# Performance work log

Hardware: AMD Instinct MI355X
Metric: run time of the kernel (lower is better)

## Reference

```python
import jax, jax.numpy as jnp
import numpy as np

B, N = 16384, 20
F = 128          # n_node_features = n_neighbors_features = embed_dim
T = 100          # time_dim
E = 128          # n_edge_features
H = 2            # n_head
OUT = 128        # output_dimension
KEY_DIM = F + T + E  # 356


def setup_inputs() -> dict:
    key = jax.random.key(0)
    ks = jax.random.split(key, 24)
    s = 0.02
    inp = {
        "src_node_features": jax.random.normal(ks[0], (B, F), jnp.float32),
        "neighbors_features": jax.random.normal(ks[1], (B, N, F), jnp.float32),
        "neighbors_time_features": jax.random.normal(ks[2], (B, N, T), jnp.float32),
        "edge_features": jax.random.normal(ks[3], (B, N, E), jnp.float32),
        "neighbors_padding_mask": jax.random.randint(ks[4], (B, N), 0, 2).astype(bool),
        "weights": jax.random.uniform(ks[5], (B, N), jnp.float32),
        # transform: Linear(key_dim -> F)
        "Wt": jax.random.normal(ks[6], (F, KEY_DIM), jnp.float32) * s,
        "bt": jnp.zeros((F,), jnp.float32),
        # MultiheadAttention projections (embed_dim = kdim = vdim = F)
        "Wq": jax.random.normal(ks[7], (F, F), jnp.float32) * s,
        "bq": jnp.zeros((F,), jnp.float32),
        "Wk": jax.random.normal(ks[8], (F, F), jnp.float32) * s,
        "bk": jnp.zeros((F,), jnp.float32),
        "Wv": jax.random.normal(ks[9], (F, F), jnp.float32) * s,
        "bv": jnp.zeros((F,), jnp.float32),
        "Wo": jax.random.normal(ks[10], (F, F), jnp.float32) * s,
        "bo": jnp.zeros((F,), jnp.float32),
        # MergeLayer: fc1(query_dim + F -> F), fc2(F -> OUT)
        "W1": jax.random.normal(ks[11], (F, F + F), jnp.float32) * s,
        "b1": jnp.zeros((F,), jnp.float32),
        "W2": jax.random.normal(ks[12], (OUT, F), jnp.float32) * s,
        "b2": jnp.zeros((OUT,), jnp.float32),
    }
    return inp


def _gat_forward(src, nbr, timef, edgef, w, mask,
                 Wt, bt, Wq, bq, Wk, bk, Wv, bv, Wo, bo, W1, b1, W2, b2):
    b, f = src.shape
    dh = f // H
    scale = 1.0 / jnp.sqrt(jnp.asarray(dh, src.dtype))
    # key = transform(cat([nbr, edge, time])) * weights  -> [B,N,F]
    k_in = jnp.concatenate([nbr, edgef, timef], axis=2)
    keyv = (jnp.einsum('bnk,fk->bnf', k_in, Wt) + bt) * w[:, :, None]
    # invalid-neighborhood fixup: rows fully padded get their first slot unmasked
    invalid = mask.all(axis=1, keepdims=True)           # [B,1]
    mask = mask.at[:, 0].set(jnp.where(invalid[:, 0], False, mask[:, 0]))
    # projections (query_len = 1)
    q = (src @ Wq.T + bq).reshape(b, H, dh)             # [B,H,dh]
    k = (keyv @ Wk.T + bk).reshape(b, N, H, dh)         # [B,N,H,dh]
    v = (keyv @ Wv.T + bv).reshape(b, N, H, dh)
    scores = jnp.einsum('bhd,bnhd->bhn', q, k) * scale  # [B,H,N]
    scores = jnp.where(mask[:, None, :], -jnp.inf, scores)
    attn = jax.nn.softmax(scores, axis=-1)
    ctx = jnp.einsum('bhn,bnhd->bhd', attn, v).reshape(b, f)
    out = ctx @ Wo.T + bo                               # [B,F]
    out = jnp.where(invalid, jnp.asarray(0.0, out.dtype), out)
    out = jax.nn.relu(out)
    # MergeLayer: fc2(relu(fc1(cat([attn_out, src]))))
    hmid = jax.nn.relu(jnp.concatenate([out, src], axis=1) @ W1.T + b1)
    return hmid @ W2.T + b2


def reference(src_node_features, neighbors_features, neighbors_time_features,
              edge_features, neighbors_padding_mask, weights,
              Wt, bt, Wq, bq, Wk, bk, Wv, bv, Wo, bo, W1, b1, W2, b2):
    return _gat_forward(src_node_features, neighbors_features,
                        neighbors_time_features, edge_features, weights,
                        neighbors_padding_mask,
                        Wt, bt, Wq, bq, Wk, bk, Wv, bv, Wo, bo, W1, b1, W2, b2)
```

## Files before the change

### kernel.cpp

```cpp
#include <hip/hip_runtime.h>
#include <math.h>

#define NN 20
#define FF 128
#define TT 100
#define EE 128
#define KD 356

typedef unsigned int u32;
typedef unsigned short u16;
typedef unsigned long long u64;
typedef __attribute__((ext_vector_type(4))) float f32x4;
typedef __attribute__((ext_vector_type(8))) short s16x8;
typedef __attribute__((ext_vector_type(4))) u32 u32x4;

__device__ __forceinline__ u16 f2b(float f) {
    u32 u = __float_as_uint(f);
    u32 r = u + 0x7FFFu + ((u >> 16) & 1u);
    return (u16)(r >> 16);
}
__device__ __forceinline__ float b2f(u16 h) { return __uint_as_float(((u32)h) << 16); }
__device__ __forceinline__ float blo(u32 u){ return __uint_as_float(u << 16); }
__device__ __forceinline__ float bhi(u32 u){ return __uint_as_float(u & 0xFFFF0000u); }
__device__ __forceinline__ u32 pk2(float a, float b){ return (u32)f2b(a) | ((u32)f2b(b) << 16); }
__device__ __forceinline__ u32 cvtpk(float a, float b){
    u32 d; asm("v_cvt_pk_bf16_f32 %0, %1, %2" : "=v"(d) : "v"(a), "v"(b)); return d;
}


__global__ void prep_fuse(const float* __restrict__ Wt, const float* __restrict__ bt,
                          const float* __restrict__ Wk, const float* __restrict__ Wv,
                          const u32* __restrict__ maskw,
                          float* __restrict__ wkt, float* __restrict__ wvt,
                          float* __restrict__ kfb, float* __restrict__ vfb, int* __restrict__ flagp)
{
    const int blk = blockIdx.x, t = threadIdx.x;
    if (blk < KD) {
        __shared__ float col[FF];
        col[t] = Wt[t * KD + blk];
        __syncthreads();
        float ak = 0.f, av = 0.f;
        for (int j = 0; j < FF; ++j) {
            float c = col[j];
            ak = fmaf(Wk[t * FF + j], c, ak);
            av = fmaf(Wv[t * FF + j], c, av);
        }
        wkt[blk * FF + t] = ak;
        wvt[blk * FF + t] = av;
    } else if (blk == KD) {
        float ak = 0.f, av = 0.f;
        for (int j = 0; j < FF; ++j) {
            float c = bt[j];
            ak = fmaf(Wk[t * FF + j], c, ak);
            av = fmaf(Wv[t * FF + j], c, av);
        }
        kfb[t] = ak; vfb[t] = av;
    } else {
        int any = 0;
        for (int i = t; i < 8192; i += 128) any |= (maskw[i] > 1u) ? 1 : 0;
        any = __any(any) ? 1 : 0;
        __shared__ int red[2];
        if ((t & 63) == 0) red[t >> 6] = any;
        __syncthreads();
        if (t == 0) *flagp = (red[0] | red[1]) ? 1 : 0;
    }
}

__global__ void prep_pack_v4(const float* __restrict__ wkt, const float* __restrict__ wvt,
                             const float* __restrict__ Wq, const float* __restrict__ Wo,
                             const float* __restrict__ W1, const float* __restrict__ W2,
                             u16* __restrict__ kvB, u16* __restrict__ wqI, u16* __restrict__ woI,
                             u16* __restrict__ w1I, u16* __restrict__ w2I)
{
    const int id = blockIdx.x * 256 + threadIdx.x;
    if (id < 196608) {
        int chunk = id >> 9, e = id & 511;
        int ln = e >> 3, ee = e & 7;
        int kt = chunk >> 4, nb = chunk & 15;
        int k = kt * 32 + (ln >> 4) * 8 + ee;
        int n = nb * 16 + (ln & 15);
        float v = 0.f;
        if (k < KD) v = (n < FF) ? wkt[k * FF + n] : wvt[k * FF + (n - FF)];
        kvB[id] = f2b(v);
    } else if (id < 215040) {
        int e = id - 196608; int rem = e % 9216;
        int n = rem / 72, kk = rem % 72; int k = (e / 9216) * 64 + kk;
        wqI[e] = f2b(kk < 64 ? Wq[n * FF + k] : 0.f);
    } else if (id < 233472) {
        int e = id - 215040; int rem = e % 9216;
        int n = rem / 72, kk = rem % 72; int k = (e / 9216) * 64 + kk;
        woI[e] = f2b(kk < 64 ? Wo[n * FF + k] : 0.f);
    } else if (id < 270336) {
        int e = id - 233472; int rem = e % 9216;
        int n = rem / 72, kk = rem % 72; int k = (e / 9216) * 64 + kk;
        w1I[e] = f2b(kk < 64 ? W1[n * 2 * FF + k] : 0.f);
    } else if (id < 288768) {
        int e = id - 270336; int rem = e % 9216;
        int n = rem / 72, kk = rem % 72; int k = (e / 9216) * 64 + kk;
        w2I[e] = f2b(kk < 64 ? W2[n * FF + k] : 0.f);
    }
}

__global__ __launch_bounds__(512) void kv_attn_fused7(
    const float* __restrict__ nbr, const float* __restrict__ edg, const float* __restrict__ tmf,
    const float* __restrict__ wgt, const float* __restrict__ bk, const float* __restrict__ bv,
    const u16* __restrict__ kvB, const float* __restrict__ kfb, const float* __restrict__ vfb,
    const u16* __restrict__ Qg, const void* __restrict__ maskp, const int* __restrict__ flagp,
    u16* __restrict__ ctxout, unsigned char* __restrict__ flags)
{
    __shared__ __align__(16) u16 smem[15680];
    char* sb = (char*)smem;
    float* p_lds = (float*)(sb + 30720);
    u16* kls = (u16*)sb;

    const int tid = threadIdx.x;
    const int lane = tid & 63, wave = tid >> 6;
    const int wn = wave;
    const int Mbase = blockIdx.x * 80;
    const int Bbase = blockIdx.x * 4;
    const int kg = lane >> 4, l16 = lane & 15;

    f32x4 acc[5][2] = {};
    s16x8 br[2][2];
    f32x4 tl[5];

    #define STAGE_CHUNK(C, KT) do {                                                         \
        int row_ = (C) * 8 + (lane >> 3);                                                   \
        int x_ = (lane & 7) ^ (row_ & 7);                                                   \
        const float* g_;                                                                    \
        if ((KT) < 4)      g_ = nbr + (size_t)(Mbase + row_) * 128 + (KT) * 32 + x_ * 4;    \
        else if ((KT) < 8) g_ = edg + (size_t)(Mbase + row_) * 128 + ((KT)-4) * 32 + x_ * 4;\
        else               g_ = tmf + (size_t)(Mbase + row_) * 100 + ((KT)-8) * 32 + x_ * 4;\
        __builtin_amdgcn_global_load_lds((const __attribute__((address_space(1))) u32*)g_,  \
            (__attribute__((address_space(3))) u32*)(sb + ((KT)%3)*10240 + (C)*1024), 16, 0, 0); \
    } while (0)

    #define STAGE(KT) do {                                                                  \
        STAGE_CHUNK(wave, KT);                                                              \
        if (wave < 2) STAGE_CHUNK(8 + wave, KT);                                            \
    } while (0)

    #define LOADB(KT) do {                                                                  \
        br[(KT)&1][0] = *(const s16x8*)(kvB + (size_t)((KT)*16 + wn*2 + 0)*512 + lane*8);   \
        br[(KT)&1][1] = *(const s16x8*)(kvB + (size_t)((KT)*16 + wn*2 + 1)*512 + lane*8);   \
    } while (0)

    #define NV1(KT) ((KT)==0?6:((KT)==1?8:((KT)==2?10:((KT)<=8?8:((KT)==9?7:6)))))
    #define NV2(KT) ((KT)==0?8:((KT)==1?10:((KT)==2?12:((KT)<=8?10:((KT)==9?8:6)))))

    #pragma unroll
    for (int mt = 0; mt < 5; ++mt)
        tl[mt] = *(const f32x4*)(tmf + (size_t)(Mbase + mt * 16 + l16) * 100 + 96);
    STAGE(0); STAGE(1); STAGE(2);
    LOADB(0); LOADB(1);

    #define GITER(KT) do {                                                                  \
        if ((KT) <= 10) {                                                                   \
            if (wave < 2) { asm volatile("s_waitcnt vmcnt(%0)" :: "i"(NV2(KT)) : "memory"); }\
            else          { asm volatile("s_waitcnt vmcnt(%0)" :: "i"(NV1(KT)) : "memory"); }\
            __builtin_amdgcn_s_barrier();                                                   \
            __builtin_amdgcn_sched_barrier(0);                                              \
        }                                                                                   \
        s16x8 af[5];                                                                        \
        _Pragma("unroll")                                                                   \
        for (int mt = 0; mt < 5; ++mt) {                                                    \
            f32x4 lo, hi;                                                                   \
            if ((KT) <= 10) {                                                               \
                int r_ = mt * 16 + l16; int sw_ = r_ & 7; int y0_ = kg * 2;                 \
                const char* bp_ = sb + ((KT)%3)*10240 + r_ * 128;                           \
                lo = *(const f32x4*)(bp_ + ((y0_ ^ sw_) << 4));                             \
                hi = *(const f32x4*)(bp_ + (((y0_+1) ^ sw_) << 4));                         \
            } else {                                                                        \
                lo = (kg == 0) ? tl[mt] : (f32x4){0.f,0.f,0.f,0.f};                         \
                hi = (f32x4){0.f,0.f,0.f,0.f};                                              \
            }                                                                               \
            u32x4 q_;                                                                       \
            q_.x = cvtpk(lo.x, lo.y); q_.y = cvtpk(lo.z, lo.w);                             \
            q_.z = cvtpk(hi.x, hi.y); q_.w = cvtpk(hi.z, hi.w);                             \
            af[mt] = __builtin_bit_cast(s16x8, q_);                                         \
        }                                                                                   \
        _Pragma("unroll")                                                                   \
        for (int mt = 0; mt < 5; ++mt) {                                                    \
            acc[mt][0] = __builtin_amdgcn_mfma_f32_16x16x32_bf16(af[mt], br[(KT)&1][0], acc[mt][0], 0, 0, 0); \
            acc[mt][1] = __builtin_amdgcn_mfma_f32_16x16x32_bf16(af[mt], br[(KT)&1][1], acc[mt][1], 0, 0, 0); \
        }                                                                                   \
        if ((KT) <= 10) {                                                                   \
            asm volatile("s_waitcnt lgkmcnt(0)" ::: "memory");                              \
            __builtin_amdgcn_s_barrier();                                                   \
            __builtin_amdgcn_sched_barrier(0);                                              \
            if ((KT) <= 7) STAGE((KT)+3);                                                   \
            if ((KT)+2 <= 11) LOADB((KT)+2);                                                \
        }                                                                                   \
    } while (0)

    GITER(0); GITER(1); GITER(2);  GITER(3);
    GITER(4); GITER(5); GITER(6);  GITER(7);
    GITER(8); GITER(9); GITER(10); GITER(11);
    #undef GITER
    #undef STAGE
    #undef STAGE_CHUNK
    #undef LOADB

    __syncthreads();

    const int rg4 = (lane >> 4) * 4;
    if (wn < 4) {
        #pragma unroll
        for (int mt = 0; mt < 5; ++mt) {
            const int r0 = mt * 16 + rg4;
            float w4v[4];
            #pragma unroll
            for (int i = 0; i < 4; ++i) w4v[i] = wgt[Mbase + r0 + i];
            #pragma unroll
            for (int nt = 0; nt < 2; ++nt) {
                const int c = wn * 32 + nt * 16 + l16;
                const float fb = kfb[c], bb = bk[c];
                #pragma unroll
                for (int i = 0; i < 4; ++i)
                    kls[(r0 + i) * 132 + c] = f2b(fmaf(acc[mt][nt][i] + fb, w4v[i], bb));
            }
        }
    } else {
        #pragma unroll
        for (int mt = 0; mt < 5; ++mt) {
            const int r0 = mt * 16 + rg4;
            float w4v[4];
            #pragma unroll
            for (int i = 0; i < 4; ++i) w4v[i] = wgt[Mbase + r0 + i];
            #pragma unroll
            for (int nt = 0; nt < 2; ++nt) {
                const int c = (wn - 4) * 32 + nt * 16 + l16;
                const float fb = vfb[c], bb = bv[c];
                #pragma unroll
                for (int i = 0; i < 4; ++i)
                    acc[mt][nt][i] = fmaf(acc[mt][nt][i] + fb, w4v[i], bb);
            }
        }
    }
    __syncthreads();

    const int lb = wave >> 1, h = wave & 1;
    const int brow = Bbase + lb;
    {
        const int flagv = *flagp;
        bool mybit = false;
        if (lane < NN) {
            if (flagv) mybit = ((const unsigned char*)maskp)[brow * NN + lane] != 0;
            else       mybit = ((const int*)maskp)[brow * NN + lane] != 0;
        }
        u64 bal = __ballot(mybit);
        u32 mb = (u32)(bal & 0xFFFFFull);
        const bool invalid = (mb == 0xFFFFFu);
        if (invalid) mb &= ~1u;
        if (h == 0 && lane == 0) flags[brow] = invalid ? 1 : 0;

        const int n = lane & 31;
        float s = -INFINITY;
        if (lane < 32 && n < NN) {
            const u16* kr = kls + (lb * NN + n) * 132 + h * 64;
            const u16* qr = Qg + (size_t)brow * 128 + h * 64;
            float d = 0.f;
            #pragma unroll
            for (int dc = 0; dc < 16; ++dc) {
                uint2 kw = *(const uint2*)(kr + dc * 4);
                uint2 qw = *(const uint2*)(qr + dc * 4);
                d = fmaf(blo(kw.x), blo(qw.x), d);  d = fmaf(bhi(kw.x), bhi(qw.x), d);
                d = fmaf(blo(kw.y), blo(qw.y), d);  d = fmaf(bhi(kw.y), bhi(qw.y), d);
            }
            s = ((mb >> n) & 1u) ? -INFINITY : d * 0.125f;
        }
        float mx = s;
        #pragma unroll
        for (int off = 16; off; off >>= 1) mx = fmaxf(mx, __shfl_xor(mx, off, 32));
        float e = (lane < 32 && n < NN) ? expf(s - mx) : 0.f;
        float sum = e;
        #pragma unroll
        for (int off = 16; off; off >>= 1) sum += __shfl_xor(sum, off, 32);
        if (lane < NN) p_lds[wave * NN + lane] = e / sum;
    }
    __syncthreads();

    if (wn >= 4) {
        #pragma unroll
        for (int mt = 0; mt < 5; ++mt) {
            const int r0 = mt * 16 + rg4;
            #pragma unroll
            for (int nt = 0; nt < 2; ++nt) {
                const int c = (wn - 4) * 32 + nt * 16 + l16;
                #pragma unroll
                for (int i = 0; i < 4; ++i)
                    kls[(r0 + i) * 132 + c] = f2b(acc[mt][nt][i]);
            }
        }
    }
    __syncthreads();

    {
        float cacc = 0.f;
        #pragma unroll
        for (int n2 = 0; n2 < NN; ++n2) {
            float pn = p_lds[wave * NN + n2];
            cacc = fmaf(pn, b2f(kls[(lb * NN + n2) * 132 + h * 64 + lane]), cacc);
        }
        ctxout[(size_t)brow * 128 + h * 64 + lane] = f2b(cacc);
    }
}

#define GM_Q 0

template<int MODE>
__global__ __launch_bounds__(256) void gemm_small(
    const void* __restrict__ Asrc, const float* __restrict__ Asrc2,
    const u16* __restrict__ Bimg, const float* __restrict__ bias,
    const unsigned char* __restrict__ flags, void* __restrict__ outp)
{
    __shared__ u16 lA[64 * 72];
    __shared__ u16 lB[128 * 72];
    const int tid = threadIdx.x;
    const int Mbase = blockIdx.x * 64;
    const int lane = tid & 63, wave = tid >> 6;
    const int wm = wave >> 1, wn = wave & 1;
    const int row = tid >> 2, cg = tid & 3;

    f32x4 acc[2][4] = {};
    const size_t r = (size_t)(Mbase + row);

    for (int kt = 0; kt < 2; ++kt) {
        {
            const float* ap = (const float*)Asrc + r * 128 + kt * 64 + cg * 16;
            f32x4 x0 = *(const f32x4*)ap,       x1 = *(const f32x4*)(ap + 4);
            f32x4 x2 = *(const f32x4*)(ap + 8), x3 = *(const f32x4*)(ap + 12);
            *(uint4*)(&lA[row * 72 + cg * 16])     = make_uint4(pk2(x0.x,x0.y), pk2(x0.z,x0.w), pk2(x1.x,x1.y), pk2(x1.z,x1.w));
            *(uint4*)(&lA[row * 72 + cg * 16 + 8]) = make_uint4(pk2(x2.x,x2.y), pk2(x2.z,x2.w), pk2(x3.x,x3.y), pk2(x3.z,x3.w));
        }
        for (int c = wave; c < 18; c += 4) {
            const char* g = (const char*)Bimg + (size_t)kt * 18432 + c * 1024 + lane * 16;
            char* l = (char*)lB + c * 1024;
            __builtin_amdgcn_global_load_lds((const __attribute__((address_space(1))) u32*)g,
                                             (__attribute__((address_space(3))) u32*)l, 16, 0, 0);
        }
        __syncthreads();
        #pragma unroll
        for (int ks = 0; ks < 2; ++ks) {
            int kk = ks * 32 + (lane >> 4) * 8;
            s16x8 a[2], b[4];
            #pragma unroll
            for (int mt = 0; mt < 2; ++mt)
                a[mt] = *(const s16x8*)(&lA[(wm * 32 + mt * 16 + (lane & 15)) * 72 + kk]);
            #pragma unroll
            for (int nt = 0; nt < 4; ++nt)
                b[nt] = *(const s16x8*)(&lB[(wn * 64 + nt * 16 + (lane & 15)) * 72 + kk]);
            #pragma unroll
            for (int mt = 0; mt < 2; ++mt)
                #pragma unroll
                for (int nt = 0; nt < 4; ++nt)
                    acc[mt][nt] = __builtin_amdgcn_mfma_f32_16x16x32_bf16(a[mt], b[nt], acc[mt][nt], 0, 0, 0);
        }
        __syncthreads();
    }

    #pragma unroll
    for (int mt = 0; mt < 2; ++mt) {
        #pragma unroll
        for (int nt = 0; nt < 4; ++nt) {
            int colg = wn * 64 + nt * 16 + (lane & 15);
            float bb = bias[colg];
            #pragma unroll
            for (int i = 0; i < 4; ++i) {
                int rg = Mbase + wm * 32 + mt * 16 + (lane >> 4) * 4 + i;
                ((u16*)outp)[(size_t)rg * 128 + colg] = f2b(acc[mt][nt][i] + bb);
            }
        }
    }
}

__global__ __launch_bounds__(256) void gemm_tail(
    const u16* __restrict__ ctx, const float* __restrict__ src,
    const u16* __restrict__ woI, const u16* __restrict__ w1I, const u16* __restrict__ w2I,
    const float* __restrict__ bo, const float* __restrict__ b1, const float* __restrict__ b2,
    const unsigned char* __restrict__ flags, float* __restrict__ outp)
{
    __shared__ u16 lA[64 * 72];
    __shared__ u16 lB[128 * 72];
    __shared__ u16 s_a[64 * 136];
    const int tid = threadIdx.x;
    const int Mbase = blockIdx.x * 64;
    const int lane = tid & 63, wave = tid >> 6;
    const int wm = wave >> 1, wn = wave & 1;
    const int row = tid >> 2, cg = tid & 3;
    const size_t r = (size_t)(Mbase + row);

    #define STAGEB(IMG, KT) do {                                                            \
        for (int c_ = wave; c_ < 18; c_ += 4) {                                             \
            const char* g_ = (const char*)(IMG) + (size_t)(KT) * 18432 + c_ * 1024 + lane * 16; \
            char* l_ = (char*)lB + c_ * 1024;                                               \
            __builtin_amdgcn_global_load_lds((const __attribute__((address_space(1))) u32*)g_, \
                                             (__attribute__((address_space(3))) u32*)l_, 16, 0, 0); \
        }                                                                                   \
    } while (0)

    #define MFMA_STEP(ASRC, ASTRIDE, KOFF) do {                                             \
        _Pragma("unroll")                                                                   \
        for (int ks_ = 0; ks_ < 2; ++ks_) {                                                 \
            int kk_ = ks_ * 32 + (lane >> 4) * 8;                                           \
            s16x8 a_[2], b_[4];                                                             \
            _Pragma("unroll")                                                               \
            for (int mt_ = 0; mt_ < 2; ++mt_)                                               \
                a_[mt_] = *(const s16x8*)(&(ASRC)[(wm * 32 + mt_ * 16 + (lane & 15)) * (ASTRIDE) + (KOFF) + kk_]); \
            _Pragma("unroll")                                                               \
            for (int nt_ = 0; nt_ < 4; ++nt_)                                               \
                b_[nt_] = *(const s16x8*)(&lB[(wn * 64 + nt_ * 16 + (lane & 15)) * 72 + kk_]); \
            _Pragma("unroll")                                                               \
            for (int mt_ = 0; mt_ < 2; ++mt_)                                               \
                _Pragma("unroll")                                                           \
                for (int nt_ = 0; nt_ < 4; ++nt_)                                           \
                    acc[mt_][nt_] = __builtin_amdgcn_mfma_f32_16x16x32_bf16(a_[mt_], b_[nt_], acc[mt_][nt_], 0, 0, 0); \
        }                                                                                   \
    } while (0)

    f32x4 acc[2][4];

    #pragma unroll
    for (int mt = 0; mt < 2; ++mt)
        #pragma unroll
        for (int nt = 0; nt < 4; ++nt) acc[mt][nt] = (f32x4){0.f,0.f,0.f,0.f};

    for (int kt = 0; kt < 2; ++kt) {
        {
            const u16* ap = ctx + r * 128 + kt * 64 + cg * 16;
            *(uint4*)(&lA[row * 72 + cg * 16])     = *(const uint4*)ap;
            *(uint4*)(&lA[row * 72 + cg * 16 + 8]) = *(const uint4*)(ap + 8);
        }
        STAGEB(woI, kt);
        __syncthreads();
        MFMA_STEP(lA, 72, 0);
        __syncthreads();
    }
    #pragma unroll
    for (int mt = 0; mt < 2; ++mt) {
        #pragma unroll
        for (int nt = 0; nt < 4; ++nt) {
            int colg = wn * 64 + nt * 16 + (lane & 15);
            float bb = bo[colg];
            #pragma unroll
            for (int i = 0; i < 4; ++i) {
                int rl = wm * 32 + mt * 16 + (lane >> 4) * 4 + i;
                float val = acc[mt][nt][i] + bb;
                if (flags[Mbase + rl]) val = 0.f;
                s_a[rl * 136 + colg] = f2b(fmaxf(val, 0.f));
            }
        }
    }
    __syncthreads();

    #pragma unroll
    for (int mt = 0; mt < 2; ++mt)
        #pragma unroll
        for (int nt = 0; nt < 4; ++nt) acc[mt][nt] = (f32x4){0.f,0.f,0.f,0.f};

    for (int kt = 0; kt < 4; ++kt) {
        if (kt >= 2) {
            const float* ap = src + r * 128 + (kt - 2) * 64 + cg * 16;
            f32x4 x0 = *(const f32x4*)ap,       x1 = *(const f32x4*)(ap + 4);
            f32x4 x2 = *(const f32x4*)(ap + 8), x3 = *(const f32x4*)(ap + 12);
            *(uint4*)(&lA[row * 72 + cg * 16])     = make_uint4(pk2(x0.x,x0.y), pk2(x0.z,x0.w), pk2(x1.x,x1.y), pk2(x1.z,x1.w));
            *(uint4*)(&lA[row * 72 + cg * 16 + 8]) = make_uint4(pk2(x2.x,x2.y), pk2(x2.z,x2.w), pk2(x3.x,x3.y), pk2(x3.z,x3.w));
        }
        STAGEB(w1I, kt);
        __syncthreads();
        if (kt < 2) MFMA_STEP(s_a, 136, kt * 64);
        else        MFMA_STEP(lA, 72, 0);
        __syncthreads();
    }
    #pragma unroll
    for (int mt = 0; mt < 2; ++mt) {
        #pragma unroll
        for (int nt = 0; nt < 4; ++nt) {
            int colg = wn * 64 + nt * 16 + (lane & 15);
            float bb = b1[colg];
            #pragma unroll
            for (int i = 0; i < 4; ++i) {
                int rl = wm * 32 + mt * 16 + (lane >> 4) * 4 + i;
                s_a[rl * 136 + colg] = f2b(fmaxf(acc[mt][nt][i] + bb, 0.f));
            }
        }
    }
    __syncthreads();

    #pragma unroll
    for (int mt = 0; mt < 2; ++mt)
        #pragma unroll
        for (int nt = 0; nt < 4; ++nt) acc[mt][nt] = (f32x4){0.f,0.f,0.f,0.f};

    for (int kt = 0; kt < 2; ++kt) {
        STAGEB(w2I, kt);
        __syncthreads();
        MFMA_STEP(s_a, 136, kt * 64);
        __syncthreads();
    }
    #pragma unroll
    for (int mt = 0; mt < 2; ++mt) {
        #pragma unroll
        for (int nt = 0; nt < 4; ++nt) {
            int colg = wn * 64 + nt * 16 + (lane & 15);
            float bb = b2[colg];
            #pragma unroll
            for (int i = 0; i < 4; ++i) {
                int rg = Mbase + wm * 32 + mt * 16 + (lane >> 4) * 4 + i;
                outp[(size_t)rg * 128 + colg] = acc[mt][nt][i] + bb;
            }
        }
    }
    #undef STAGEB
    #undef MFMA_STEP
}


__global__ void prep_pack_r2(const float* __restrict__ wkt, const float* __restrict__ wvt,
                             const float* __restrict__ Wq, const float* __restrict__ Wo,
                             const float* __restrict__ W1, const float* __restrict__ W2,
                             u16* __restrict__ bpack, u32* __restrict__ wq2, u32* __restrict__ wo2,
                             u32* __restrict__ w12, u32* __restrict__ w22)
{
    const int id = blockIdx.x * 256 + threadIdx.x;
    if (id < 98304) {
        int kt = id >> 14;
        int o  = id & 16383;
        int n  = o >> 6;
        int kk = (o & 63) ^ ((n & 7) << 3);
        int k  = kt * 64 + kk;
        float v = 0.f;
        if (k < KD) v = (n < FF) ? wkt[k * FF + n] : wvt[k * FF + (n - FF)];
        bpack[id] = f2b(v);
    } else if (id < 106496) {
        int e = id - 98304; int j = e >> 6, tt = e & 63;
        wq2[e] = (u32)f2b(Wq[tt * FF + j]) | ((u32)f2b(Wq[(tt + 64) * FF + j]) << 16);
    } else if (id < 114688) {
        int e = id - 106496; int j = e >> 6, tt = e & 63;
        wo2[e] = (u32)f2b(Wo[tt * FF + j]) | ((u32)f2b(Wo[(tt + 64) * FF + j]) << 16);
    } else if (id < 131072) {
        int e = id - 114688; int j = e >> 6, tt = e & 63;
        w12[e] = (u32)f2b(W1[tt * 2 * FF + j]) | ((u32)f2b(W1[(tt + 64) * 2 * FF + j]) << 16);
    } else if (id < 139264) {
        int e = id - 131072; int j = e >> 6, tt = e & 63;
        w22[e] = (u32)f2b(W2[tt * FF + j]) | ((u32)f2b(W2[(tt + 64) * FF + j]) << 16);
    }
}

__global__ __launch_bounds__(512) void kv_gemm_r2(
    const float* __restrict__ nbr, const float* __restrict__ edg, const float* __restrict__ tmf,
    const float* __restrict__ wgt, const float* __restrict__ bk, const float* __restrict__ bv,
    const u16* __restrict__ bpack, const float* __restrict__ kfb, const float* __restrict__ vfb,
    u16* __restrict__ kvout)
{
    __shared__ u16 lA[128 * 64];
    __shared__ u16 lB[256 * 64];
    const int tid = threadIdx.x;
    const int Mbase = blockIdx.x * 128;
    const int lane = tid & 63, wave = tid >> 6;
    const int wm = wave >> 2, wn = wave & 3;

    f32x4 acc[4][4] = {};
    const int rq = tid >> 4;
    const int cq = tid & 15;

    for (int kt = 0; kt < 6; ++kt) {
        #pragma unroll
        for (int i = 0; i < 4; ++i) {
            int row = rq + i * 32;
            size_t r = (size_t)(Mbase + row);
            f32x4 v;
            if (kt < 2)       v = *(const f32x4*)(nbr + r * 128 + kt * 64 + cq * 4);
            else if (kt < 4)  v = *(const f32x4*)(edg + r * 128 + (kt - 2) * 64 + cq * 4);
            else if (kt == 4) v = *(const f32x4*)(tmf + r * 100 + cq * 4);
            else if (cq < 9)  v = *(const f32x4*)(tmf + r * 100 + 64 + cq * 4);
            else              v = (f32x4){0.f, 0.f, 0.f, 0.f};
            int off = row * 64 + ((cq * 4) ^ ((row & 7) << 3));
            *(uint2*)(&lA[off]) = make_uint2(pk2(v.x, v.y), pk2(v.z, v.w));
        }
        #pragma unroll
        for (int i = 0; i < 4; ++i) {
            int boff = wave * 4096 + i * 1024;
            const char* g = (const char*)bpack + (size_t)kt * 32768 + boff + lane * 16;
            char* l = (char*)lB + boff;
            __builtin_amdgcn_global_load_lds((const __attribute__((address_space(1))) u32*)g,
                                             (__attribute__((address_space(3))) u32*)l, 16, 0, 0);
        }
        __syncthreads();
        #pragma unroll
        for (int ks = 0; ks < 2; ++ks) {
            int kk = ks * 32 + (lane >> 4) * 8;
            s16x8 a[4], b[4];
            #pragma unroll
            for (int mt = 0; mt < 4; ++mt) {
                int m = wm * 64 + mt * 16 + (lane & 15);
                a[mt] = *(const s16x8*)(&lA[m * 64 + (kk ^ ((m & 7) << 3))]);
            }
            #pragma unroll
            for (int nt = 0; nt < 4; ++nt) {
                int n = wn * 64 + nt * 16 + (lane & 15);
                b[nt] = *(const s16x8*)(&lB[n * 64 + (kk ^ ((n & 7) << 3))]);
            }
            #pragma unroll
            for (int mt = 0; mt < 4; ++mt)
                #pragma unroll
                for (int nt = 0; nt < 4; ++nt)
                    acc[mt][nt] = __builtin_amdgcn_mfma_f32_16x16x32_bf16(a[mt], b[nt], acc[mt][nt], 0, 0, 0);
        }
// ... 112 lines not shown
            o1 = fmaf(bhi(u), cj, o1);
        }
        if (invalid) { o0 = 0.f; o1 = 0.f; }
        o0 = fmaxf(o0, 0.f); o1 = fmaxf(o1, 0.f);
        s_out[t] = o0; s_out[64 + t] = o1;
    }
    __syncthreads();

    {
        float h0 = b1[t], h1 = b1[64 + t];
        for (int j = 0; j < FF; ++j) {
            u32 u = w12[j * 64 + t];
            float xj = s_out[j];
            h0 = fmaf(blo(u), xj, h0);
            h1 = fmaf(bhi(u), xj, h1);
        }
        for (int j = 0; j < FF; ++j) {
            u32 u = w12[(FF + j) * 64 + t];
            float xj = s_src[j];
            h0 = fmaf(blo(u), xj, h0);
            h1 = fmaf(bhi(u), xj, h1);
        }
        h0 = fmaxf(h0, 0.f); h1 = fmaxf(h1, 0.f);
        s_h[t] = h0; s_h[64 + t] = h1;
    }
    __syncthreads();

    {
        float f0 = b2[t], f1 = b2[64 + t];
        for (int j = 0; j < FF; ++j) {
            u32 u = w22[j * 64 + t];
            float hj = s_h[j];
            f0 = fmaf(blo(u), hj, f0);
            f1 = fmaf(bhi(u), hj, f1);
        }
        out[(size_t)b * FF + t] = f0;
        out[(size_t)b * FF + 64 + t] = f1;
    }
}


#define FB_WKT  0
#define FB_WVT  (FB_WKT + KD*FF)
#define FB_KB   (FB_WVT + KD*FF)
#define FB_VB   (FB_KB + FF)
#define FB_WQT  (FB_VB + FF)
#define FB_WOT  (FB_WQT + FF*FF)
#define FB_W1T  (FB_WOT + FF*FF)
#define FB_W2T  (FB_W1T + 2*FF*FF)
#define FB_FLAG (FB_W2T + FF*FF)

__global__ void gat_prep_fb(const float* __restrict__ Wt, const float* __restrict__ bt,
                            const float* __restrict__ Wq, const float* __restrict__ Wk,
                            const float* __restrict__ Wv, const float* __restrict__ Wo,
                            const float* __restrict__ W1, const float* __restrict__ W2,
                            const u32* __restrict__ maskw, float* __restrict__ ws)
{
    const int blk = blockIdx.x;
    const int t = threadIdx.x;
    if (blk < KD) {
        __shared__ float col[FF];
        col[t] = Wt[t * KD + blk];
        __syncthreads();
        float ak = 0.f, av = 0.f;
        for (int j = 0; j < FF; ++j) {
            float c = col[j];
            ak = fmaf(Wk[t * FF + j], c, ak);
            av = fmaf(Wv[t * FF + j], c, av);
        }
        ws[FB_WKT + blk * FF + t] = ak;
        ws[FB_WVT + blk * FF + t] = av;
    } else if (blk == KD) {
        float ak = 0.f, av = 0.f;
        for (int j = 0; j < FF; ++j) {
            float c = bt[j];
            ak = fmaf(Wk[t * FF + j], c, ak);
            av = fmaf(Wv[t * FF + j], c, av);
        }
        ws[FB_KB + t] = ak;
        ws[FB_VB + t] = av;
    } else if (blk == KD + 1) {
        int any = 0;
        for (int i = t; i < 8192; i += 128) any |= (maskw[i] > 1u) ? 1 : 0;
        any = __any(any) ? 1 : 0;
        __shared__ int red[2];
        if ((t & 63) == 0) red[t >> 6] = any;
        __syncthreads();
        if (t == 0) ((int*)ws)[FB_FLAG] = (red[0] | red[1]) ? 1 : 0;
    } else {
        int id = (blk - (KD + 2)) * 128 + t;
        if (id < FF * FF) {
            int k = id >> 7, f = id & 127;
            ws[FB_WQT + id] = Wq[f * FF + k];
        } else if (id < 2 * FF * FF) {
            int e = id - FF * FF; int k = e >> 7, f = e & 127;
            ws[FB_WOT + e] = Wo[f * FF + k];
        } else if (id < 4 * FF * FF) {
            int e = id - 2 * FF * FF; int j = e >> 7, f = e & 127;
            ws[FB_W1T + e] = W1[f * (2 * FF) + j];
        } else if (id < 5 * FF * FF) {
            int e = id - 4 * FF * FF; int k = e >> 7, f = e & 127;
            ws[FB_W2T + e] = W2[f * FF + k];
        }
    }
}

__global__ __launch_bounds__(64) void gat_main_fb(
    const float* __restrict__ src, const float* __restrict__ nbr,
    const float* __restrict__ tmf, const float* __restrict__ edg,
    const void* __restrict__ maskp, const float* __restrict__ wgt,
    const float* __restrict__ bq, const float* __restrict__ bk,
    const float* __restrict__ bv, const float* __restrict__ bo,
    const float* __restrict__ b1, const float* __restrict__ b2,
    const float* __restrict__ ws, float* __restrict__ out)
{
    const int b = blockIdx.x;
    const int t = threadIdx.x;
    __shared__ __align__(16) float kin[KD * NN];
    __shared__ float s_src[FF], s_q[FF], s_ctx[FF], s_out[FF], s_h[FF];
    __shared__ float s_w[NN], s_sc[2 * NN];

    const int flag = ((const int*)ws)[FB_FLAG];
    bool mybit = false;
    if (t < NN) {
        if (flag) mybit = ((const unsigned char*)maskp)[b * NN + t] != 0;
        else      mybit = ((const int*)maskp)[b * NN + t] != 0;
    }
    u64 bal = __ballot(mybit);
    u32 mb = (u32)(bal & 0xFFFFFull);
    const bool invalid = (mb == 0xFFFFFu);
    if (invalid) mb &= ~1u;

    s_src[t] = src[(size_t)b * FF + t];
    s_src[t + 64] = src[(size_t)b * FF + 64 + t];
    if (t < NN) s_w[t] = wgt[(size_t)b * NN + t];

    for (int idx = t; idx < NN * FF; idx += 64) {
        int n = idx >> 7, j = idx & 127;
        kin[j * NN + n]         = nbr[((size_t)b * NN + n) * FF + j];
        kin[(128 + j) * NN + n] = edg[((size_t)b * NN + n) * EE + j];
    }
    for (int idx = t; idx < NN * TT; idx += 64) {
        int n = idx / TT, j = idx - n * TT;
        kin[(256 + j) * NN + n] = tmf[((size_t)b * NN + n) * TT + j];
    }
    __syncthreads();

    const float* wkt = ws + FB_WKT;
    const float* wvt = ws + FB_WVT;
    float ak0[NN], ak1[NN], av0[NN], av1[NN];
#pragma unroll
    for (int n = 0; n < NN; ++n) { ak0[n] = 0.f; ak1[n] = 0.f; av0[n] = 0.f; av1[n] = 0.f; }
    for (int k = 0; k < KD; ++k) {
        float wk0 = wkt[k * FF + t],      wk1 = wkt[k * FF + 64 + t];
        float wv0 = wvt[k * FF + t],      wv1 = wvt[k * FF + 64 + t];
        const float4* cp = (const float4*)(kin + k * NN);
        float4 ca = cp[0], cb = cp[1], cc = cp[2], cd = cp[3], ce = cp[4];
        const float c[NN] = { ca.x, ca.y, ca.z, ca.w,  cb.x, cb.y, cb.z, cb.w,
                              cc.x, cc.y, cc.z, cc.w,  cd.x, cd.y, cd.z, cd.w,
                              ce.x, ce.y, ce.z, ce.w };
#pragma unroll
        for (int n = 0; n < NN; ++n) {
            ak0[n] = fmaf(wk0, c[n], ak0[n]);
            ak1[n] = fmaf(wk1, c[n], ak1[n]);
            av0[n] = fmaf(wv0, c[n], av0[n]);
            av1[n] = fmaf(wv1, c[n], av1[n]);
        }
    }
    __syncthreads();

    float* kls = kin;
    float* vls = kin + NN * 129;
    {
        const float kb0 = ws[FB_KB + t], kb1 = ws[FB_KB + 64 + t];
        const float vb0 = ws[FB_VB + t], vb1 = ws[FB_VB + 64 + t];
        const float k0b = bk[t], k1b = bk[64 + t];
        const float v0b = bv[t], v1b = bv[64 + t];
#pragma unroll
        for (int n = 0; n < NN; ++n) {
            float wn = s_w[n];
            kls[n * 129 + t]      = fmaf(wn, ak0[n] + kb0, k0b);
            kls[n * 129 + 64 + t] = fmaf(wn, ak1[n] + kb1, k1b);
            vls[n * 129 + t]      = fmaf(wn, av0[n] + vb0, v0b);
            vls[n * 129 + 64 + t] = fmaf(wn, av1[n] + vb1, v1b);
        }
    }
    {
        const float* wqT = ws + FB_WQT;
        float q0 = bq[t], q1 = bq[64 + t];
        for (int j = 0; j < FF; ++j) {
            float sj = s_src[j];
            q0 = fmaf(wqT[j * FF + t], sj, q0);
            q1 = fmaf(wqT[j * FF + 64 + t], sj, q1);
        }
        s_q[t] = q0; s_q[64 + t] = q1;
    }
    __syncthreads();

    if (t < 2 * NN) {
        int h = t / NN, n = t - (t / NN) * NN;
        const float* kr = kls + n * 129 + h * 64;
        const float* qr = s_q + h * 64;
        float s = 0.f;
#pragma unroll
        for (int d = 0; d < 64; ++d) s = fmaf(qr[d], kr[d], s);
        s *= 0.125f;
        s_sc[t] = ((mb >> n) & 1u) ? -INFINITY : s;
    }
    __syncthreads();
    if (t < 2) {
        float mx = -INFINITY;
        for (int n = 0; n < NN; ++n) mx = fmaxf(mx, s_sc[t * NN + n]);
        float e[NN]; float sum = 0.f;
        for (int n = 0; n < NN; ++n) { e[n] = expf(s_sc[t * NN + n] - mx); sum += e[n]; }
        float inv = 1.f / sum;
        for (int n = 0; n < NN; ++n) s_sc[t * NN + n] = e[n] * inv;
    }
    __syncthreads();

    {
        float c0 = 0.f, c1 = 0.f;
#pragma unroll
        for (int n = 0; n < NN; ++n) {
            c0 = fmaf(s_sc[n],      vls[n * 129 + t],      c0);
            c1 = fmaf(s_sc[NN + n], vls[n * 129 + 64 + t], c1);
        }
        s_ctx[t] = c0; s_ctx[64 + t] = c1;
    }
    __syncthreads();

    {
        const float* woT = ws + FB_WOT;
        float o0 = bo[t], o1 = bo[64 + t];
        for (int j = 0; j < FF; ++j) {
            float cj = s_ctx[j];
            o0 = fmaf(woT[j * FF + t], cj, o0);
            o1 = fmaf(woT[j * FF + 64 + t], cj, o1);
        }
        if (invalid) { o0 = 0.f; o1 = 0.f; }
        o0 = fmaxf(o0, 0.f); o1 = fmaxf(o1, 0.f);
        s_out[t] = o0; s_out[64 + t] = o1;
    }
    __syncthreads();

    {
        const float* w1T = ws + FB_W1T;
        float h0 = b1[t], h1 = b1[64 + t];
        for (int j = 0; j < FF; ++j) {
            float xj = s_out[j];
            h0 = fmaf(w1T[j * FF + t], xj, h0);
            h1 = fmaf(w1T[j * FF + 64 + t], xj, h1);
        }
        for (int j = 0; j < FF; ++j) {
            float xj = s_src[j];
            h0 = fmaf(w1T[(FF + j) * FF + t], xj, h0);
            h1 = fmaf(w1T[(FF + j) * FF + 64 + t], xj, h1);
        }
        h0 = fmaxf(h0, 0.f); h1 = fmaxf(h1, 0.f);
        s_h[t] = h0; s_h[64 + t] = h1;
    }
    __syncthreads();

    {
        const float* w2T = ws + FB_W2T;
        float f0 = b2[t], f1 = b2[64 + t];
        for (int j = 0; j < FF; ++j) {
            float hj = s_h[j];
            f0 = fmaf(w2T[j * FF + t], hj, f0);
            f1 = fmaf(w2T[j * FF + 64 + t], hj, f1);
        }
        out[(size_t)b * FF + t] = f0;
        out[(size_t)b * FF + 64 + t] = f1;
    }
}


extern "C" void kernel_launch(void* const* d_in, const int* in_sizes, int n_in,
                              void* d_out, int out_size, void* d_ws, size_t ws_size,
                              hipStream_t stream)
{
    const float* src = (const float*)d_in[0];
    const float* nbr = (const float*)d_in[1];
    const float* tmf = (const float*)d_in[2];
    const float* edg = (const float*)d_in[3];
    const void*  msk = d_in[4];
    const float* wgt = (const float*)d_in[5];
    const float* Wt  = (const float*)d_in[6];
    const float* bt  = (const float*)d_in[7];
    const float* Wq  = (const float*)d_in[8];
    const float* bq  = (const float*)d_in[9];
    const float* Wk  = (const float*)d_in[10];
    const float* bk  = (const float*)d_in[11];
    const float* Wv  = (const float*)d_in[12];
    const float* bv  = (const float*)d_in[13];
    const float* Wo  = (const float*)d_in[14];
    const float* bo  = (const float*)d_in[15];
    const float* W1  = (const float*)d_in[16];
    const float* b1  = (const float*)d_in[17];
    const float* W2  = (const float*)d_in[18];
    const float* b2  = (const float*)d_in[19];

    const int B = in_sizes[0] / FF;
    const size_t M = (size_t)B * NN;

    size_t o1 = 0;
    size_t t1_qa   = o1; o1 += (size_t)B * 256;
    size_t t1_ch   = o1; o1 += (size_t)B * 256;
    size_t t1_kvB  = o1; o1 += 393216;
    size_t t1_wqI  = o1; o1 += 36864;
    size_t t1_woI  = o1; o1 += 36864;
    size_t t1_w1I  = o1; o1 += 73728;
    size_t t1_w2I  = o1; o1 += 36864;
    size_t t1_wkt  = o1; o1 += (size_t)KD * FF * 4;
    size_t t1_wvt  = o1; o1 += (size_t)KD * FF * 4;
    size_t t1_kfb  = o1; o1 += 512;
    size_t t1_vfb  = o1; o1 += 512;
    size_t t1_flg  = o1; o1 += (size_t)B;
    o1 = (o1 + 255) & ~(size_t)255;
    size_t t1_flag = o1; o1 += 64;
    const size_t need1 = o1;

    size_t o2 = 0;
    size_t t2_kv    = o2; o2 += M * 512;
    size_t t2_bpack = o2; o2 += 98304ull * 2;
    size_t t2_wkt   = o2; o2 += (size_t)KD * FF * 4;
    size_t t2_wvt   = o2; o2 += (size_t)KD * FF * 4;
    size_t t2_kfb   = o2; o2 += 512;
    size_t t2_vfb   = o2; o2 += 512;
    size_t t2_wq2   = o2; o2 += 32768;
    size_t t2_wo2   = o2; o2 += 32768;
    size_t t2_w12   = o2; o2 += 65536;
    size_t t2_w22   = o2; o2 += 32768;
    size_t t2_flag  = o2; o2 += 64;
    const size_t need2 = o2;

    char* w = (char*)d_ws;

    if (ws_size >= need1 && (B % 64) == 0) {
        u16*   qa    = (u16*)(w + t1_qa);
        u16*   ch    = (u16*)(w + t1_ch);
        u16*   kvB   = (u16*)(w + t1_kvB);
        u16*   wqI   = (u16*)(w + t1_wqI);
        u16*   woI   = (u16*)(w + t1_woI);
        u16*   w1I   = (u16*)(w + t1_w1I);
        u16*   w2I   = (u16*)(w + t1_w2I);
        float* wktp  = (float*)(w + t1_wkt);
        float* wvtp  = (float*)(w + t1_wvt);
        float* kfb   = (float*)(w + t1_kfb);
        float* vfb   = (float*)(w + t1_vfb);
        unsigned char* flg = (unsigned char*)(w + t1_flg);
        int*   flagp = (int*)(w + t1_flag);

        prep_fuse<<<dim3(KD + 2), dim3(128), 0, stream>>>(Wt, bt, Wk, Wv,
            (const u32*)msk, wktp, wvtp, kfb, vfb, flagp);
        prep_pack_v4<<<dim3(1128), dim3(256), 0, stream>>>(wktp, wvtp, Wq, Wo, W1, W2,
            kvB, wqI, woI, w1I, w2I);
        gemm_small<GM_Q><<<dim3(B / 64), dim3(256), 0, stream>>>(
            (const void*)src, nullptr, wqI, bq, nullptr, (void*)qa);
        kv_attn_fused7<<<dim3(B / 4), dim3(512), 0, stream>>>(
            nbr, edg, tmf, wgt, bk, bv, kvB, kfb, vfb, qa, msk, flagp, ch, flg);
        gemm_tail<<<dim3(B / 64), dim3(256), 0, stream>>>(
            ch, src, woI, w1I, w2I, bo, b1, b2, flg, (float*)d_out);
    } else if (ws_size >= need2 && (M % 128) == 0) {
        u16*   kvp   = (u16*)(w + t2_kv);
        u16*   bpack = (u16*)(w + t2_bpack);
        float* wktp  = (float*)(w + t2_wkt);
        float* wvtp  = (float*)(w + t2_wvt);
        float* kfb   = (float*)(w + t2_kfb);
        float* vfb   = (float*)(w + t2_vfb);
        u32*   wq2   = (u32*)(w + t2_wq2);
        u32*   wo2   = (u32*)(w + t2_wo2);
        u32*   w12   = (u32*)(w + t2_w12);
        u32*   w22   = (u32*)(w + t2_w22);
        int*   flagp = (int*)(w + t2_flag);

        prep_fuse<<<dim3(KD + 2), dim3(128), 0, stream>>>(Wt, bt, Wk, Wv,
            (const u32*)msk, wktp, wvtp, kfb, vfb, flagp);
        prep_pack_r2<<<dim3(544), dim3(256), 0, stream>>>(wktp, wvtp, Wq, Wo, W1, W2,
            bpack, wq2, wo2, w12, w22);
        kv_gemm_r2<<<dim3((int)(M / 128)), dim3(512), 0, stream>>>(
            nbr, edg, tmf, wgt, bk, bv, bpack, kfb, vfb, kvp);
        gat_attn_r2<<<dim3(B), dim3(64), 0, stream>>>(
            src, msk, bq, bo, b1, b2, kvp, wq2, wo2, w12, w22, flagp, (float*)d_out);
    } else {
        float* ws = (float*)d_ws;
        gat_prep_fb<<<dim3(KD + 2 + 640), dim3(128), 0, stream>>>(
            Wt, bt, Wq, Wk, Wv, Wo, W1, W2, (const u32*)msk, ws);
        gat_main_fb<<<dim3(B), dim3(64), 0, stream>>>(
            src, nbr, tmf, edg, msk, wgt, bq, bk, bv, bo, b1, b2, ws, (float*)d_out);
    }
}
```

Before: 205.2 us.

## Make fused KV-attention kernel persistent over groups with cross-group prefetch

The fused KV projection and attention kernel now handles NG=8 groups of 4 batch rows per block instead of one, looping over groups. The LDS staging for the next group's GEMM tiles is issued right after the current group's GEMM, so those loads overlap with the current group's attention epilogue. The K/V tile is moved to a separate LDS region so the staging buffers are not overwritten. This cuts block launch count and hides global-load latency, but uses more LDS per block (about 52KB), which may lower occupancy, and leaves 512 blocks to cover the GPU.

```diff
diff --git a/kernel.cpp b/kernel.cpp
--- a/kernel.cpp
+++ b/kernel.cpp
@@ -25,6 +25,11 @@
 __device__ __forceinline__ u32 pk2(float a, float b){ return (u32)f2b(a) | ((u32)f2b(b) << 16); }
 __device__ __forceinline__ u32 cvtpk(float a, float b){
     u32 d; asm("v_cvt_pk_bf16_f32 %0, %1, %2" : "=v"(d) : "v"(a), "v"(b)); return d;
+}
+__device__ __forceinline__ void lgkm_barrier() {
+    asm volatile("s_waitcnt lgkmcnt(0)" ::: "memory");
+    __builtin_amdgcn_s_barrier();
+    asm volatile("" ::: "memory");
 }
 
 
@@ -101,43 +106,47 @@
     }
 }
 
-__global__ __launch_bounds__(512) void kv_attn_fused7(
+template<int NG>
+__global__ __launch_bounds__(512) void kv_attn_fused8(
     const float* __restrict__ nbr, const float* __restrict__ edg, const float* __restrict__ tmf,
     const float* __restrict__ wgt, const float* __restrict__ bk, const float* __restrict__ bv,
     const u16* __restrict__ kvB, const float* __restrict__ kfb, const float* __restrict__ vfb,
     const u16* __restrict__ Qg, const void* __restrict__ maskp, const int* __restrict__ flagp,
     u16* __restrict__ ctxout, unsigned char* __restrict__ flags)
 {
-    __shared__ __align__(16) u16 smem[15680];
+    __shared__ __align__(16) u16 smem[26240];
     char* sb = (char*)smem;
-    float* p_lds = (float*)(sb + 30720);
-    u16* kls = (u16*)sb;
+    u16* kls = (u16*)(sb + 30720);
+    float* p_lds = (float*)(sb + 51840);
 
     const int tid = threadIdx.x;
     const int lane = tid & 63, wave = tid >> 6;
     const int wn = wave;
-    const int Mbase = blockIdx.x * 80;
-    const int Bbase = blockIdx.x * 4;
     const int kg = lane >> 4, l16 = lane & 15;
-
-    f32x4 acc[5][2] = {};
+    const int rg4 = (lane >> 4) * 4;
+    const int lb = wave >> 1, h = wave & 1;
+    const int flagv = *flagp;
+
+    int Mbase = blockIdx.x * NG * 80;
+
+    f32x4 acc[5][2];
     s16x8 br[2][2];
     f32x4 tl[5];
 
-    #define STAGE_CHUNK(C, KT) do {                                                         \
+    #define STAGE_CHUNK(C, KT, MB) do {                                                     \
         int row_ = (C) * 8 + (lane >> 3);                                                   \
         int x_ = (lane & 7) ^ (row_ & 7);                                                   \
         const float* g_;                                                                    \
-        if ((KT) < 4)      g_ = nbr + (size_t)(Mbase + row_) * 128 + (KT) * 32 + x_ * 4;    \
-        else if ((KT) < 8) g_ = edg + (size_t)(Mbase + row_) * 128 + ((KT)-4) * 32 + x_ * 4;\
-        else               g_ = tmf + (size_t)(Mbase + row_) * 100 + ((KT)-8) * 32 + x_ * 4;\
+        if ((KT) < 4)      g_ = nbr + (size_t)((MB) + row_) * 128 + (KT) * 32 + x_ * 4;     \
+        else if ((KT) < 8) g_ = edg + (size_t)((MB) + row_) * 128 + ((KT)-4) * 32 + x_ * 4; \
+        else               g_ = tmf + (size_t)((MB) + row_) * 100 + ((KT)-8) * 32 + x_ * 4; \
         __builtin_amdgcn_global_load_lds((const __attribute__((address_space(1))) u32*)g_,  \
             (__attribute__((address_space(3))) u32*)(sb + ((KT)%3)*10240 + (C)*1024), 16, 0, 0); \
     } while (0)
 
-    #define STAGE(KT) do {                                                                  \
-        STAGE_CHUNK(wave, KT);                                                              \
-        if (wave < 2) STAGE_CHUNK(8 + wave, KT);                                            \
+    #define STAGE(KT, MB) do {                                                              \
+        STAGE_CHUNK(wave, KT, MB);                                                          \
+        if (wave < 2) STAGE_CHUNK(8 + wave, KT, MB);                                        \
     } while (0)
 
     #define LOADB(KT) do {                                                                  \
@@ -145,14 +154,16 @@
         br[(KT)&1][1] = *(const s16x8*)(kvB + (size_t)((KT)*16 + wn*2 + 1)*512 + lane*8);   \
     } while (0)
 
+    #define PREFETCH(MB) do {                                                               \
+        _Pragma("unroll")                                                                   \
+        for (int mt_ = 0; mt_ < 5; ++mt_)                                                   \
+            tl[mt_] = *(const f32x4*)(tmf + (size_t)((MB) + mt_ * 16 + l16) * 100 + 96);    \
+        STAGE(0, MB); STAGE(1, MB); STAGE(2, MB);                                           \
+        LOADB(0); LOADB(1);                                                                 \
+    } while (0)
+
     #define NV1(KT) ((KT)==0?6:((KT)==1?8:((KT)==2?10:((KT)<=8?8:((KT)==9?7:6)))))
     #define NV2(KT) ((KT)==0?8:((KT)==1?10:((KT)==2?12:((KT)<=8?10:((KT)==9?8:6)))))
-
-    #pragma unroll
-    for (int mt = 0; mt < 5; ++mt)
-        tl[mt] = *(const f32x4*)(tmf + (size_t)(Mbase + mt * 16 + l16) * 100 + 96);
-    STAGE(0); STAGE(1); STAGE(2);
-    LOADB(0); LOADB(1);
 
     #define GITER(KT) do {                                                                  \
         if ((KT) <= 10) {                                                                   \
@@ -188,122 +199,134 @@
             asm volatile("s_waitcnt lgkmcnt(0)" ::: "memory");                              \
             __builtin_amdgcn_s_barrier();                                                   \
             __builtin_amdgcn_sched_barrier(0);                                              \
-            if ((KT) <= 7) STAGE((KT)+3);                                                   \
+            if ((KT) <= 7) STAGE((KT)+3, Mbase);                                            \
             if ((KT)+2 <= 11) LOADB((KT)+2);                                                \
         }                                                                                   \
     } while (0)
 
-    GITER(0); GITER(1); GITER(2);  GITER(3);
-    GITER(4); GITER(5); GITER(6);  GITER(7);
-    GITER(8); GITER(9); GITER(10); GITER(11);
+    PREFETCH(Mbase);
+
+    #pragma unroll 1
+    for (int g = 0; g < NG; ++g) {
+        #pragma unroll
+        for (int mt = 0; mt < 5; ++mt) {
+            acc[mt][0] = (f32x4){0.f,0.f,0.f,0.f};
+            acc[mt][1] = (f32x4){0.f,0.f,0.f,0.f};
+        }
+
+        GITER(0); GITER(1); GITER(2);  GITER(3);
+        GITER(4); GITER(5); GITER(6);  GITER(7);
+        GITER(8); GITER(9); GITER(10); GITER(11);
+
+        if (g + 1 < NG) PREFETCH(Mbase + 80);
+
+        if (wn < 4) {
+            #pragma unroll
+            for (int mt = 0; mt < 5; ++mt) {
+                const int r0 = mt * 16 + rg4;
+                float w4v[4];
+                #pragma unroll
+                for (int i = 0; i < 4; ++i) w4v[i] = wgt[Mbase + r0 + i];
+                #pragma unroll
+                for (int nt = 0; nt < 2; ++nt) {
+                    const int c = wn * 32 + nt * 16 + l16;
+                    const float fb = kfb[c], bb = bk[c];
+                    #pragma unroll
+                    for (int i = 0; i < 4; ++i)
+                        kls[(r0 + i) * 132 + c] = f2b(fmaf(acc[mt][nt][i] + fb, w4v[i], bb));
+                }
+            }
+        } else {
+            #pragma unroll
+            for (int mt = 0; mt < 5; ++mt) {
+                const int r0 = mt * 16 + rg4;
+                float w4v[4];
+                #pragma unroll
+                for (int i = 0; i < 4; ++i) w4v[i] = wgt[Mbase + r0 + i];
+                #pragma unroll
+                for (int nt = 0; nt < 2; ++nt) {
+                    const int c = (wn - 4) * 32 + nt * 16 + l16;
+                    const float fb = vfb[c], bb = bv[c];
+                    #pragma unroll
+                    for (int i = 0; i < 4; ++i)
+                        acc[mt][nt][i] = fmaf(acc[mt][nt][i] + fb, w4v[i], bb);
+                }
+            }
+        }
+        lgkm_barrier();
+
+        const int brow = (blockIdx.x * NG + g) * 4 + lb;
+        {
+            bool mybit = false;
+            if (lane < NN) {
+                if (flagv) mybit = ((const unsigned char*)maskp)[brow * NN + lane] != 0;
+                else       mybit = ((const int*)maskp)[brow * NN + lane] != 0;
+            }
+            u64 bal = __ballot(mybit);
+            u32 mb = (u32)(bal & 0xFFFFFull);
+            const bool invalid = (mb == 0xFFFFFu);
+            if (invalid) mb &= ~1u;
+            if (h == 0 && lane == 0) flags[brow] = invalid ? 1 : 0;
+
+            const int n = lane & 31;
+            float s = -INFINITY;
+            if (lane < 32 && n < NN) {
+                const u16* kr = kls + (lb * NN + n) * 132 + h * 64;
+                const u16* qr = Qg + (size_t)brow * 128 + h * 64;
+                float d = 0.f;
+                #pragma unroll
+                for (int dc = 0; dc < 16; ++dc) {
+                    uint2 kw = *(const uint2*)(kr + dc * 4);
+                    uint2 qw = *(const uint2*)(qr + dc * 4);
+                    d = fmaf(blo(kw.x), blo(qw.x), d);  d = fmaf(bhi(kw.x), bhi(qw.x), d);
+                    d = fmaf(blo(kw.y), blo(qw.y), d);  d = fmaf(bhi(kw.y), bhi(qw.y), d);
+                }
+                s = ((mb >> n) & 1u) ? -INFINITY : d * 0.125f;
+            }
+            float mx = s;
+            #pragma unroll
+            for (int off = 16; off; off >>= 1) mx = fmaxf(mx, __shfl_xor(mx, off, 32));
+            float e = (lane < 32 && n < NN) ? expf(s - mx) : 0.f;
+            float sum = e;
+            #pragma unroll
+            for (int off = 16; off; off >>= 1) sum += __shfl_xor(sum, off, 32);
+            if (lane < NN) p_lds[wave * NN + lane] = e / sum;
+        }
+        lgkm_barrier();
+
+        if (wn >= 4) {
+            #pragma unroll
+            for (int mt = 0; mt < 5; ++mt) {
+                const int r0 = mt * 16 + rg4;
+                #pragma unroll
+                for (int nt = 0; nt < 2; ++nt) {
+                    const int c = (wn - 4) * 32 + nt * 16 + l16;
+                    #pragma unroll
+                    for (int i = 0; i < 4; ++i)
+                        kls[(r0 + i) * 132 + c] = f2b(acc[mt][nt][i]);
+                }
+            }
+        }
+        lgkm_barrier();
+
+        {
+            float cacc = 0.f;
+            #pragma unroll
+            for (int n2 = 0; n2 < NN; ++n2) {
+                float pn = p_lds[wave * NN + n2];
+                cacc = fmaf(pn, b2f(kls[(lb * NN + n2) * 132 + h * 64 + lane]), cacc);
+            }
+            ctxout[(size_t)brow * 128 + h * 64 + lane] = f2b(cacc);
+        }
+        Mbase += 80;
+    }
     #undef GITER
+    #undef PREFETCH
     #undef STAGE
     #undef STAGE_CHUNK
     #undef LOADB
-
-    __syncthreads();
-
-    const int rg4 = (lane >> 4) * 4;
-    if (wn < 4) {
-        #pragma unroll
-        for (int mt = 0; mt < 5; ++mt) {
-            const int r0 = mt * 16 + rg4;
-            float w4v[4];
-            #pragma unroll
-            for (int i = 0; i < 4; ++i) w4v[i] = wgt[Mbase + r0 + i];
-            #pragma unroll
-            for (int nt = 0; nt < 2; ++nt) {
-                const int c = wn * 32 + nt * 16 + l16;
-                const float fb = kfb[c], bb = bk[c];
-                #pragma unroll
-                for (int i = 0; i < 4; ++i)
-                    kls[(r0 + i) * 132 + c] = f2b(fmaf(acc[mt][nt][i] + fb, w4v[i], bb));
-            }
-        }
-    } else {
-        #pragma unroll
-        for (int mt = 0; mt < 5; ++mt) {
-            const int r0 = mt * 16 + rg4;
-            float w4v[4];
-            #pragma unroll
-            for (int i = 0; i < 4; ++i) w4v[i] = wgt[Mbase + r0 + i];
-            #pragma unroll
-            for (int nt = 0; nt < 2; ++nt) {
-                const int c = (wn - 4) * 32 + nt * 16 + l16;
-                const float fb = vfb[c], bb = bv[c];
-                #pragma unroll
-                for (int i = 0; i < 4; ++i)
-                    acc[mt][nt][i] = fmaf(acc[mt][nt][i] + fb, w4v[i], bb);
-            }
-        }
-    }
-    __syncthreads();
-
-    const int lb = wave >> 1, h = wave & 1;
-    const int brow = Bbase + lb;
-    {
-        const int flagv = *flagp;
-        bool mybit = false;
-        if (lane < NN) {
-            if (flagv) mybit = ((const unsigned char*)maskp)[brow * NN + lane] != 0;
-            else       mybit = ((const int*)maskp)[brow * NN + lane] != 0;
-        }
-        u64 bal = __ballot(mybit);
-        u32 mb = (u32)(bal & 0xFFFFFull);
-        const bool invalid = (mb == 0xFFFFFu);
-        if (invalid) mb &= ~1u;
-        if (h == 0 && lane == 0) flags[brow] = invalid ? 1 : 0;
-
-        const int n = lane & 31;
-        float s = -INFINITY;
-        if (lane < 32 && n < NN) {
-            const u16* kr = kls + (lb * NN + n) * 132 + h * 64;
-            const u16* qr = Qg + (size_t)brow * 128 + h * 64;
-            float d = 0.f;
-            #pragma unroll
-            for (int dc = 0; dc < 16; ++dc) {
-                uint2 kw = *(const uint2*)(kr + dc * 4);
-                uint2 qw = *(const uint2*)(qr + dc * 4);
-                d = fmaf(blo(kw.x), blo(qw.x), d);  d = fmaf(bhi(kw.x), bhi(qw.x), d);
-                d = fmaf(blo(kw.y), blo(qw.y), d);  d = fmaf(bhi(kw.y), bhi(qw.y), d);
-            }
-            s = ((mb >> n) & 1u) ? -INFINITY : d * 0.125f;
-        }
-        float mx = s;
-        #pragma unroll
-        for (int off = 16; off; off >>= 1) mx = fmaxf(mx, __shfl_xor(mx, off, 32));
-        float e = (lane < 32 && n < NN) ? expf(s - mx) : 0.f;
-        float sum = e;
-        #pragma unroll
-        for (int off = 16; off; off >>= 1) sum += __shfl_xor(sum, off, 32);
-        if (lane < NN) p_lds[wave * NN + lane] = e / sum;
-    }
-    __syncthreads();
-
-    if (wn >= 4) {
-        #pragma unroll
-        for (int mt = 0; mt < 5; ++mt) {
-            const int r0 = mt * 16 + rg4;
-            #pragma unroll
-            for (int nt = 0; nt < 2; ++nt) {
-                const int c = (wn - 4) * 32 + nt * 16 + l16;
-                #pragma unroll
-                for (int i = 0; i < 4; ++i)
-                    kls[(r0 + i) * 132 + c] = f2b(acc[mt][nt][i]);
-            }
-        }
-    }
-    __syncthreads();
-
-    {
-        float cacc = 0.f;
-        #pragma unroll
-        for (int n2 = 0; n2 < NN; ++n2) {
-            float pn = p_lds[wave * NN + n2];
-            cacc = fmaf(pn, b2f(kls[(lb * NN + n2) * 132 + h * 64 + lane]), cacc);
-        }
-        ctxout[(size_t)brow * 128 + h * 64 + lane] = f2b(cacc);
-    }
+    #undef NV1
+    #undef NV2
 }
 
 #define GM_Q 0
@@ -1022,6 +1045,7 @@
 
     const int B = in_sizes[0] / FF;
     const size_t M = (size_t)B * NN;
+    constexpr int NG = 8;
 
     size_t o1 = 0;
     size_t t1_qa   = o1; o1 += (size_t)B * 256;
@@ -1056,7 +1080,7 @@
 
     char* w = (char*)d_ws;
 
-    if (ws_size >= need1 && (B % 64) == 0) {
+    if (ws_size >= need1 && (B % (4 * NG * 2)) == 0) {
         u16*   qa    = (u16*)(w + t1_qa);
         u16*   ch    = (u16*)(w + t1_ch);
         u16*   kvB   = (u16*)(w + t1_kvB);
@@ -1077,7 +1101,7 @@
             kvB, wqI, woI, w1I, w2I);
         gemm_small<GM_Q><<<dim3(B / 64), dim3(256), 0, stream>>>(
             (const void*)src, nullptr, wqI, bq, nullptr, (void*)qa);
-        kv_attn_fused7<<<dim3(B / 4), dim3(512), 0, stream>>>(
+        kv_attn_fused8<NG><<<dim3(B / (4 * NG)), dim3(512), 0, stream>>>(
             nbr, edg, tmf, wgt, bk, bv, kvB, kfb, vfb, qa, msk, flagp, ch, flg);
         gemm_tail<<<dim3(B / 64), dim3(256), 0, stream>>>(
             ch, src, woI, w1I, w2I, bo, b1, b2, flg, (float*)d_out);
```

New measurement: 250.3 us. 1.22x slower.
